# Kernel optimization log

Hardware: AMD Instinct MI355X
Metric: run time of the kernel (lower is better)

The kernel has to match this reference:

```python
import jax, jax.numpy as jnp
import numpy as np

B, N, C = 2, 65536, 256
HEADS, DIM_HEAD, SLICE_NUM = 8, 64, 64
INNER = HEADS * DIM_HEAD


def setup_inputs() -> dict:
    key = jax.random.key(0)
    ks = jax.random.split(key, 7)
    s_in = 1.0 / np.sqrt(C)
    s_dh = 1.0 / np.sqrt(DIM_HEAD)
    return {
        "x": jax.random.normal(ks[0], (B, N, C), dtype=jnp.float32),
        "Wx": jax.random.uniform(ks[1], (C, INNER), jnp.float32, -s_in, s_in),
        "bx": jax.random.uniform(ks[2], (INNER,), jnp.float32, -s_in, s_in),
        "Wfx": jax.random.uniform(ks[3], (C, INNER), jnp.float32, -s_in, s_in),
        "bfx": jax.random.uniform(ks[4], (INNER,), jnp.float32, -s_in, s_in),
        "Wslice": jax.random.uniform(ks[5], (DIM_HEAD, SLICE_NUM), jnp.float32, -s_dh, s_dh),
        "bslice": jax.random.uniform(ks[6], (SLICE_NUM,), jnp.float32, -s_dh, s_dh),
        "temperature": jnp.ones((1, HEADS, 1, 1), dtype=jnp.float32) * 0.5,
    }


def reference(x, Wx, bx, Wfx, bfx, Wslice, bslice, temperature):
    b, n, _ = x.shape
    # Linear projections, split heads: (B, N, H*D) -> (B, H, N, D)
    px = (x @ Wx + bx).reshape(b, n, HEADS, DIM_HEAD).transpose(0, 2, 1, 3)
    fx = (x @ Wfx + bfx).reshape(b, n, HEADS, DIM_HEAD).transpose(0, 2, 1, 3)
    # Project onto slices: (B, H, N, S)
    slice_proj = px @ Wslice + bslice
    # Temperature-scaled softmax over slices
    temp = jnp.clip(temperature, 0.5, 5.0)
    slice_weights = jax.nn.softmax(slice_proj / temp, axis=-1)
    # Normalize by per-slice mass over tokens, then aggregate
    slice_norm = slice_weights.sum(axis=2)  # (B, H, S)
    normed = slice_weights / (slice_norm[:, :, None, :] + 0.01)
    slice_tokens = jnp.einsum("bhns,bhnd->bhsd", normed, fx)
    return slice_tokens
```

## Files before the change

kernel.cpp:

```cpp
#include <hip/hip_runtime.h>
#include <hip/hip_bf16.h>


typedef __attribute__((ext_vector_type(8))) short short8;
typedef __attribute__((ext_vector_type(4))) short short4v;
typedef __attribute__((ext_vector_type(4))) float float4v;

#define WPITCH 264
#define TPITCH 72

__device__ __forceinline__ unsigned short f2bf(float f) {
    union { float f; unsigned int u; } v; v.f = f;
    unsigned int r = (v.u + 0x7FFFu + ((v.u >> 16) & 1u)) >> 16;
    return (unsigned short)r;
}

__global__ void msfe_prep(const float* __restrict__ Wx, const float* __restrict__ bx,
                          const float* __restrict__ Wfx,
                          const float* __restrict__ Wslice, const float* __restrict__ bslice,
                          unsigned short* __restrict__ Wt, float* __restrict__ bc) {
    int j = blockIdx.x;
    int c = threadIdx.x;
    if (j < 512) {
        int h = j >> 6, s = j & 63;
        float acc = 0.f;
        #pragma unroll 8
        for (int d = 0; d < 64; ++d)
            acc += Wx[c * 512 + h * 64 + d] * Wslice[d * 64 + s];
        Wt[j * 256 + c] = f2bf(acc);
        if (c == 0) {
            float b = bslice[s];
            for (int d = 0; d < 64; ++d) b += bx[h * 64 + d] * Wslice[d * 64 + s];
            bc[j] = b;
        }
    } else {
        int col = j - 512;
        Wt[j * 256 + c] = f2bf(Wfx[c * 512 + col]);
    }
}

__global__ __launch_bounds__(512, 2)
void msfe_main(const float* __restrict__ x,
               const unsigned short* __restrict__ Wt,
               const float* __restrict__ bc,
               const float* __restrict__ bfx,
               const float* __restrict__ temperature,
               float* __restrict__ Tg, float* __restrict__ ng) {
    __shared__ unsigned short Ws[128 * WPITCH];
    __shared__ unsigned short Xs[64 * WPITCH];
    __shared__ unsigned short wT[64 * TPITCH];
    __shared__ unsigned short fT[64 * TPITCH];

    const int tid  = threadIdx.x;
    const int lane = tid & 63;
    const int wv   = tid >> 6;
    const int quad = lane >> 4;
    const int l16  = lane & 15;

    const int bidx = blockIdx.x;
    const int c8   = bidx & 7;
    const int ti   = (bidx >> 3) & 3;
    const int head = (bidx >> 5) & 7;
    const int rnd  = bidx >> 8;
    const int tile = rnd * 32 + c8 * 4 + ti;
    const int batch = tile >> 7;
    const long tok0 = (long)tile * 512;

    {
        int r = tid & 127;
        int part = tid >> 7;
        int grow = (r < 64) ? (head * 64 + r) : (512 + head * 64 + (r - 64));
        const short4v* src = (const short4v*)(Wt + grow * 256 + part * 64);
        short4v* dst = (short4v*)(Ws + r * WPITCH + part * 64);
        #pragma unroll
        for (int j = 0; j < 16; ++j) dst[j] = src[j];
    }

    {
        const float4v* xg = (const float4v*)(x + tok0 * 256);
        #pragma unroll
        for (int i = 0; i < 8; ++i) {
            float4v v = xg[tid + i * 512];
            int f = (tid + i * 512) * 4;
            int trow = f >> 8, col = f & 255;
            short4v p;
            p.x = (short)f2bf(v.x); p.y = (short)f2bf(v.y);
            p.z = (short)f2bf(v.z); p.w = (short)f2bf(v.w);
            *(short4v*)(Xs + trow * WPITCH + col) = p;
        }
    }

    float bcr[4], bfxr[4];
    #pragma unroll
    for (int nt = 0; nt < 4; ++nt) {
        bcr[nt]  = bc [head * 64 + nt * 16 + l16];
        bfxr[nt] = bfx[head * 64 + nt * 16 + l16];
    }
    float tmp = temperature[head];
    tmp = fminf(fmaxf(tmp, 0.5f), 5.0f);
    const float invt = 1.0f / tmp;

    float4v Tac[2];
    Tac[0] = (float4v){0.f, 0.f, 0.f, 0.f};
    Tac[1] = (float4v){0.f, 0.f, 0.f, 0.f};
    float normAcc[4] = {0.f, 0.f, 0.f, 0.f};

    const int proj = wv >> 2;
    const int tw   = wv & 3;
    const int sh   = wv & 3;
    const int dh   = wv >> 2;

    __syncthreads();

    for (int c = 0; c < 8; ++c) {
        float4v xr[8];
        if (c < 7) {
            const float4v* xg = (const float4v*)(x + (tok0 + (long)(c + 1) * 64) * 256);
            #pragma unroll
            for (int i = 0; i < 8; ++i) xr[i] = xg[tid + i * 512];
        }

        float4v acc[4];
        #pragma unroll
        for (int nt = 0; nt < 4; ++nt) acc[nt] = (float4v){0.f, 0.f, 0.f, 0.f};
        #pragma unroll
        for (int ks = 0; ks < 8; ++ks) {
            short8 a = *(const short8*)(Xs + (tw * 16 + l16) * WPITCH + ks * 32 + quad * 8);
            #pragma unroll
            for (int nt = 0; nt < 4; ++nt) {
                short8 b = *(const short8*)(Ws + (proj * 64 + nt * 16 + l16) * WPITCH + ks * 32 + quad * 8);
                acc[nt] = __builtin_amdgcn_mfma_f32_16x16x32_bf16(a, b, acc[nt], 0, 0, 0);
            }
        }

        if (proj == 0) {
            float v[4][4];
            #pragma unroll
            for (int nt = 0; nt < 4; ++nt)
                #pragma unroll
                for (int r = 0; r < 4; ++r)
                    v[nt][r] = (acc[nt][r] + bcr[nt]) * invt;
            #pragma unroll
            for (int r = 0; r < 4; ++r) {
                float m = fmaxf(fmaxf(v[0][r], v[1][r]), fmaxf(v[2][r], v[3][r]));
                m = fmaxf(m, __shfl_xor(m, 1));
                m = fmaxf(m, __shfl_xor(m, 2));
                m = fmaxf(m, __shfl_xor(m, 4));
                m = fmaxf(m, __shfl_xor(m, 8));
                float e0 = __expf(v[0][r] - m), e1 = __expf(v[1][r] - m);
                float e2 = __expf(v[2][r] - m), e3 = __expf(v[3][r] - m);
                float s = e0 + e1 + e2 + e3;
                s += __shfl_xor(s, 1); s += __shfl_xor(s, 2);
                s += __shfl_xor(s, 4); s += __shfl_xor(s, 8);
                float inv = 1.0f / s;
                v[0][r] = e0 * inv; v[1][r] = e1 * inv; v[2][r] = e2 * inv; v[3][r] = e3 * inv;
            }
            #pragma unroll
            for (int nt = 0; nt < 4; ++nt) {
                normAcc[nt] += v[nt][0] + v[nt][1] + v[nt][2] + v[nt][3];
                short4v p;
                p.x = (short)f2bf(v[nt][0]); p.y = (short)f2bf(v[nt][1]);
                p.z = (short)f2bf(v[nt][2]); p.w = (short)f2bf(v[nt][3]);
                *(short4v*)(wT + (nt * 16 + l16) * TPITCH + tw * 16 + quad * 4) = p;
            }
        } else {
            #pragma unroll
            for (int nt = 0; nt < 4; ++nt) {
                short4v p;
                p.x = (short)f2bf(acc[nt][0] + bfxr[nt]);
                p.y = (short)f2bf(acc[nt][1] + bfxr[nt]);
                p.z = (short)f2bf(acc[nt][2] + bfxr[nt]);
                p.w = (short)f2bf(acc[nt][3] + bfxr[nt]);
                *(short4v*)(fT + (nt * 16 + l16) * TPITCH + tw * 16 + quad * 4) = p;
            }
        }

        __syncthreads();

        #pragma unroll
        for (int ks = 0; ks < 2; ++ks) {
            short8 a = *(const short8*)(wT + (sh * 16 + l16) * TPITCH + ks * 32 + quad * 8);
            #pragma unroll
            for (int nt = 0; nt < 2; ++nt) {
                short8 b = *(const short8*)(fT + (dh * 32 + nt * 16 + l16) * TPITCH + ks * 32 + quad * 8);
                Tac[nt] = __builtin_amdgcn_mfma_f32_16x16x32_bf16(a, b, Tac[nt], 0, 0, 0);
            }
        }

        if (c < 7) {
            #pragma unroll
            for (int i = 0; i < 8; ++i) {
                int f = tid * 4 + i * 2048;
                int trow = f >> 8, col = f & 255;
                short4v p;
                p.x = (short)f2bf(xr[i].x); p.y = (short)f2bf(xr[i].y);
                p.z = (short)f2bf(xr[i].z); p.w = (short)f2bf(xr[i].w);
                *(short4v*)(Xs + trow * WPITCH + col) = p;
            }
        }
        __syncthreads();
    }

    const int basehs = (batch * 8 + head) * 64;
    #pragma unroll
    for (int nt = 0; nt < 2; ++nt) {
        #pragma unroll
        for (int r = 0; r < 4; ++r) {
            int s = sh * 16 + quad * 4 + r;
            int d = dh * 32 + nt * 16 + l16;
            atomicAdd(&Tg[(basehs + s) * 64 + d], Tac[nt][r]);
        }
    }
    if (wv < 4) {
        #pragma unroll
        for (int nt = 0; nt < 4; ++nt) {
            float v = normAcc[nt];
            v += __shfl_xor(v, 16);
            v += __shfl_xor(v, 32);
            if (quad == 0) atomicAdd(&ng[basehs + nt * 16 + l16], v);
        }
    }
}

__global__ void msfe_final(const float* __restrict__ Tg, const float* __restrict__ ng,
                           float* __restrict__ out) {
    int i = blockIdx.x * 256 + threadIdx.x;
    out[i] = Tg[i] / (ng[i >> 6] + 0.01f);
}

extern "C" void kernel_launch(void* const* d_in, const int* in_sizes, int n_in,
                              void* d_out, int out_size, void* d_ws, size_t ws_size,
                              hipStream_t stream) {
    const float* x       = (const float*)d_in[0];
    const float* Wx      = (const float*)d_in[1];
    const float* bx      = (const float*)d_in[2];
    const float* Wfx     = (const float*)d_in[3];
    const float* bfx     = (const float*)d_in[4];
    const float* Wslice  = (const float*)d_in[5];
    const float* bslice  = (const float*)d_in[6];
    const float* temp    = (const float*)d_in[7];

    char* ws = (char*)d_ws;
    unsigned short* Wt = (unsigned short*)ws;
    float* bc = (float*)(ws + 524288);
    float* Tg = (float*)(ws + 526336);
    float* ng = (float*)(ws + 788480);

    hipMemsetAsync(Tg, 0, 262144 + 4096, stream);

    msfe_prep<<<1024, 256, 0, stream>>>(Wx, bx, Wfx, Wslice, bslice, Wt, bc);
    msfe_main<<<2048, 512, 0, stream>>>(x, Wt, bc, bfx, temp, Tg, ng);
    msfe_final<<<256, 256, 0, stream>>>(Tg, ng, (float*)d_out);
}
```

Before: 380.7 us.

## Pre-convert x to bf16 fragment layout and keep weights in registers

```diff
diff --git a/kernel.cpp b/kernel.cpp
--- a/kernel.cpp
+++ b/kernel.cpp
@@ -14,6 +14,231 @@
     unsigned int r = (v.u + 0x7FFFu + ((v.u >> 16) & 1u)) >> 16;
     return (unsigned short)r;
 }
+
+
+__global__ void msfe_xprep(const float* __restrict__ x, unsigned short* __restrict__ xf) {
+    const int blk  = blockIdx.x;
+    const int tid  = threadIdx.x;
+    const int tw   = tid >> 6;
+    const int lane = tid & 63;
+    const int quad = lane >> 4;
+    const int l16  = lane & 15;
+    const float* xrow = x + ((long)blk * 64 + tw * 16 + l16) * 256;
+    unsigned short* ob = xf + (((long)blk * 4 + tw) * 8) * 512 + lane * 8;
+    #pragma unroll
+    for (int ks = 0; ks < 8; ++ks) {
+        const float4v* p = (const float4v*)(xrow + ks * 32 + quad * 8);
+        float4v v0 = p[0], v1 = p[1];
+        short8 o;
+        o[0] = (short)f2bf(v0.x); o[1] = (short)f2bf(v0.y);
+        o[2] = (short)f2bf(v0.z); o[3] = (short)f2bf(v0.w);
+        o[4] = (short)f2bf(v1.x); o[5] = (short)f2bf(v1.y);
+        o[6] = (short)f2bf(v1.z); o[7] = (short)f2bf(v1.w);
+        *(short8*)(ob + ks * 512) = o;
+    }
+}
+
+__global__ void msfe_prep2(const float* __restrict__ Wx, const float* __restrict__ bx,
+                           const float* __restrict__ Wfx,
+                           const float* __restrict__ Wslice, const float* __restrict__ bslice,
+                           unsigned short* __restrict__ WtF, float* __restrict__ bcv) {
+    const int b = blockIdx.x, tid = threadIdx.x;
+    if (b < 64) {
+        const int proj = b >> 5, hb = b & 31, head = hb >> 2, nt = hb & 3;
+        #pragma unroll
+        for (int p = 0; p < 2; ++p) {
+            int idx = tid + p * 256;
+            int ks = idx >> 6, l = idx & 63;
+            int quad = l >> 4, l16 = l & 15;
+            unsigned short* out = WtF + ((((long)(proj * 8 + head) * 4 + nt) * 8 + ks) * 64 + l) * 8;
+            if (proj == 0) {
+                int s = nt * 16 + l16;
+                #pragma unroll
+                for (int j = 0; j < 8; ++j) {
+                    int k = ks * 32 + quad * 8 + j;
+                    const float* wr = Wx + k * 512 + head * 64;
+                    float acc = 0.f;
+                    #pragma unroll 8
+                    for (int d = 0; d < 64; ++d)
+                        acc += wr[d] * Wslice[d * 64 + s];
+                    out[j] = f2bf(acc);
+                }
+            } else {
+                int col = head * 64 + nt * 16 + l16;
+                #pragma unroll
+                for (int j = 0; j < 8; ++j) {
+                    int k = ks * 32 + quad * 8 + j;
+                    out[j] = f2bf(Wfx[k * 512 + col]);
+                }
+            }
+        }
+    } else {
+        #pragma unroll
+        for (int p = 0; p < 2; ++p) {
+            int j = tid + p * 256;
+            int h = j >> 6, s = j & 63;
+            float bsum = bslice[s];
+            for (int d = 0; d < 64; ++d) bsum += bx[h * 64 + d] * Wslice[d * 64 + s];
+            bcv[j] = bsum;
+        }
+    }
+}
+
+__global__ __launch_bounds__(512, 2)
+void msfe_main2(const unsigned short* __restrict__ xf,
+                const unsigned short* __restrict__ WtF,
+                const float* __restrict__ bcv,
+                const float* __restrict__ bfx,
+                const float* __restrict__ temperature,
+                float* __restrict__ Tg, float* __restrict__ ng) {
+    __shared__ unsigned short wT[64 * TPITCH];
+    __shared__ unsigned short fT[64 * TPITCH];
+
+    const int tid  = threadIdx.x;
+    const int lane = tid & 63;
+    const int wv   = tid >> 6;
+    const int quad = lane >> 4;
+    const int l16  = lane & 15;
+
+    const int bidx = blockIdx.x;
+    const int c8   = bidx & 7;
+    const int ti   = (bidx >> 3) & 3;
+    const int head = (bidx >> 5) & 7;
+    const int rnd  = bidx >> 8;
+    const int tile = rnd * 32 + c8 * 4 + ti;
+    const int batch = tile >> 7;
+
+    const int proj = wv >> 2;
+    const int tw   = wv & 3;
+    const int sh   = wv & 3;
+    const int dh   = wv >> 2;
+
+    short8 wfr[4][8];
+    {
+        const unsigned short* wb = WtF + (((long)(proj * 8 + head) * 4) * 8) * 512 + lane * 8;
+        #pragma unroll
+        for (int nt = 0; nt < 4; ++nt)
+            #pragma unroll
+            for (int ks = 0; ks < 8; ++ks)
+                wfr[nt][ks] = *(const short8*)(wb + (nt * 8 + ks) * 512);
+    }
+
+    float bcr[4], bfxr[4];
+    #pragma unroll
+    for (int nt = 0; nt < 4; ++nt) {
+        bcr[nt]  = bcv[head * 64 + nt * 16 + l16];
+        bfxr[nt] = bfx[head * 64 + nt * 16 + l16];
+    }
+    float tmp = temperature[head];
+    tmp = fminf(fmaxf(tmp, 0.5f), 5.0f);
+    const float invt = 1.0f / tmp;
+
+    float4v Tac[2];
+    Tac[0] = (float4v){0.f, 0.f, 0.f, 0.f};
+    Tac[1] = (float4v){0.f, 0.f, 0.f, 0.f};
+    float normAcc[4] = {0.f, 0.f, 0.f, 0.f};
+
+    const unsigned short* xb = xf + ((long)tile * 8 * 4 * 8) * 512 + lane * 8;
+    short8 afr[8];
+    #pragma unroll
+    for (int ks = 0; ks < 8; ++ks)
+        afr[ks] = *(const short8*)(xb + ((0 * 4 + tw) * 8 + ks) * 512);
+
+    for (int c = 0; c < 8; ++c) {
+        float4v acc[4];
+        #pragma unroll
+        for (int nt = 0; nt < 4; ++nt) acc[nt] = (float4v){0.f, 0.f, 0.f, 0.f};
+        #pragma unroll
+        for (int ks = 0; ks < 8; ++ks) {
+            #pragma unroll
+            for (int nt = 0; nt < 4; ++nt)
+                acc[nt] = __builtin_amdgcn_mfma_f32_16x16x32_bf16(afr[ks], wfr[nt][ks], acc[nt], 0, 0, 0);
+        }
+
+        if (c < 7) {
+            #pragma unroll
+            for (int ks = 0; ks < 8; ++ks)
+                afr[ks] = *(const short8*)(xb + (((c + 1) * 4 + tw) * 8 + ks) * 512);
+        }
+
+        if (proj == 0) {
+            float v[4][4];
+            #pragma unroll
+            for (int nt = 0; nt < 4; ++nt)
+                #pragma unroll
+                for (int r = 0; r < 4; ++r)
+                    v[nt][r] = (acc[nt][r] + bcr[nt]) * invt;
+            #pragma unroll
+            for (int r = 0; r < 4; ++r) {
+                float m = fmaxf(fmaxf(v[0][r], v[1][r]), fmaxf(v[2][r], v[3][r]));
+                m = fmaxf(m, __shfl_xor(m, 1));
+                m = fmaxf(m, __shfl_xor(m, 2));
+                m = fmaxf(m, __shfl_xor(m, 4));
+                m = fmaxf(m, __shfl_xor(m, 8));
+                float e0 = __expf(v[0][r] - m), e1 = __expf(v[1][r] - m);
+                float e2 = __expf(v[2][r] - m), e3 = __expf(v[3][r] - m);
+                float s = e0 + e1 + e2 + e3;
+                s += __shfl_xor(s, 1); s += __shfl_xor(s, 2);
+                s += __shfl_xor(s, 4); s += __shfl_xor(s, 8);
+                float inv = 1.0f / s;
+                v[0][r] = e0 * inv; v[1][r] = e1 * inv; v[2][r] = e2 * inv; v[3][r] = e3 * inv;
+            }
+            #pragma unroll
+            for (int nt = 0; nt < 4; ++nt) {
+                normAcc[nt] += v[nt][0] + v[nt][1] + v[nt][2] + v[nt][3];
+                short4v p;
+                p.x = (short)f2bf(v[nt][0]); p.y = (short)f2bf(v[nt][1]);
+                p.z = (short)f2bf(v[nt][2]); p.w = (short)f2bf(v[nt][3]);
+                *(short4v*)(wT + (nt * 16 + l16) * TPITCH + tw * 16 + quad * 4) = p;
+            }
+        } else {
+            #pragma unroll
+            for (int nt = 0; nt < 4; ++nt) {
+                short4v p;
+                p.x = (short)f2bf(acc[nt][0] + bfxr[nt]);
+                p.y = (short)f2bf(acc[nt][1] + bfxr[nt]);
+                p.z = (short)f2bf(acc[nt][2] + bfxr[nt]);
+                p.w = (short)f2bf(acc[nt][3] + bfxr[nt]);
+                *(short4v*)(fT + (nt * 16 + l16) * TPITCH + tw * 16 + quad * 4) = p;
+            }
+        }
+
+        __syncthreads();
+
+        #pragma unroll
+        for (int ks = 0; ks < 2; ++ks) {
+            short8 a = *(const short8*)(wT + (sh * 16 + l16) * TPITCH + ks * 32 + quad * 8);
+            #pragma unroll
+            for (int nt = 0; nt < 2; ++nt) {
+                short8 b = *(const short8*)(fT + (dh * 32 + nt * 16 + l16) * TPITCH + ks * 32 + quad * 8);
+                Tac[nt] = __builtin_amdgcn_mfma_f32_16x16x32_bf16(a, b, Tac[nt], 0, 0, 0);
+            }
+        }
+
+        __syncthreads();
+    }
+
+    const int basehs = (batch * 8 + head) * 64;
+    #pragma unroll
+    for (int nt = 0; nt < 2; ++nt) {
+        #pragma unroll
+        for (int r = 0; r < 4; ++r) {
+            int s = sh * 16 + quad * 4 + r;
+            int d = dh * 32 + nt * 16 + l16;
+            atomicAdd(&Tg[(basehs + s) * 64 + d], Tac[nt][r]);
+        }
+    }
+    if (wv < 4) {
+        #pragma unroll
+        for (int nt = 0; nt < 4; ++nt) {
+            float v = normAcc[nt];
+            v += __shfl_xor(v, 16);
+            v += __shfl_xor(v, 32);
+            if (quad == 0) atomicAdd(&ng[basehs + nt * 16 + l16], v);
+        }
+    }
+}
+
 
 __global__ void msfe_prep(const float* __restrict__ Wx, const float* __restrict__ bx,
                           const float* __restrict__ Wfx,
@@ -75,7 +300,6 @@
         #pragma unroll
         for (int j = 0; j < 16; ++j) dst[j] = src[j];
     }
-
     {
         const float4v* xg = (const float4v*)(x + tok0 * 256);
         #pragma unroll
@@ -241,14 +465,29 @@
     const float* temp    = (const float*)d_in[7];
 
     char* ws = (char*)d_ws;
-    unsigned short* Wt = (unsigned short*)ws;
-    float* bc = (float*)(ws + 524288);
-    float* Tg = (float*)(ws + 526336);
-    float* ng = (float*)(ws + 788480);
-
-    hipMemsetAsync(Tg, 0, 262144 + 4096, stream);
-
-    msfe_prep<<<1024, 256, 0, stream>>>(Wx, bx, Wfx, Wslice, bslice, Wt, bc);
-    msfe_main<<<2048, 512, 0, stream>>>(x, Wt, bc, bfx, temp, Tg, ng);
-    msfe_final<<<256, 256, 0, stream>>>(Tg, ng, (float*)d_out);
-}
+    const size_t NEED = 67901440;
+
+    if (ws_size >= NEED) {
+        unsigned short* xf  = (unsigned short*)ws;
+        unsigned short* WtF = (unsigned short*)(ws + 67108864);
+        float* bc = (float*)(ws + 67633152);
+        float* Tg = (float*)(ws + 67635200);
+        float* ng = (float*)(ws + 67897344);
+
+        hipMemsetAsync(Tg, 0, 262144 + 4096, stream);
+        msfe_prep2<<<65, 256, 0, stream>>>(Wx, bx, Wfx, Wslice, bslice, WtF, bc);
+        msfe_xprep<<<2048, 256, 0, stream>>>(x, xf);
+        msfe_main2<<<2048, 512, 0, stream>>>(xf, WtF, bc, bfx, temp, Tg, ng);
+        msfe_final<<<256, 256, 0, stream>>>(Tg, ng, (float*)d_out);
+    } else {
+        unsigned short* Wt = (unsigned short*)ws;
+        float* bc = (float*)(ws + 524288);
+        float* Tg = (float*)(ws + 526336);
+        float* ng = (float*)(ws + 788480);
+
+        hipMemsetAsync(Tg, 0, 262144 + 4096, stream);
+        msfe_prep<<<1024, 256, 0, stream>>>(Wx, bx, Wfx, Wslice, bslice, Wt, bc);
+        msfe_main<<<2048, 512, 0, stream>>>(x, Wt, bc, bfx, temp, Tg, ng);
+        msfe_final<<<256, 256, 0, stream>>>(Tg, ng, (float*)d_out);
+    }
+}
```

New measurement: 390.8 us. 2.6% more time.
